# Kernel optimization log

Hardware: AMD Instinct MI355X
Metric: run time of the kernel (lower is better)

Reference implementation:

```python
import jax, jax.numpy as jnp
import numpy as np

B, L = 4096, 64
H, E, T, S = 512, 256, 256, 128
CT = T + 3            # context feature dim (term_embedding_dim + 3)
R, V = 4096, 256      # n production rules, n symbols
IN = 2 * E + 2 * T + 6 + H + S  # GRUCell input dim = 1670
NEG = -1e9


def setup_inputs() -> dict:
    key = jax.random.key(0)
    ks = jax.random.split(key, 24)
    sc = 0.02
    inp = {
        "s_tm1": jax.random.normal(ks[0], (B, H), jnp.float32),
        "a_tm1": jax.random.normal(ks[1], (B, E), jnp.float32),
        "p_t": jax.random.normal(ks[2], (B, H + E), jnp.float32),
        "symbol_idx": jax.random.randint(ks[3], (B,), 0, V, jnp.int32),
        "env_emb": jax.random.normal(ks[4], (B, L, CT), jnp.float32),
        "env_len": jax.random.randint(ks[5], (B,), 0, L, jnp.int32),
        "lc_emb": jax.random.normal(ks[6], (B, L, CT), jnp.float32),
        "lc_len": jax.random.randint(ks[7], (B,), 0, L, jnp.int32),
        # parameters
        "symbol_table": jax.random.normal(ks[8], (V, S), jnp.float32) * sc,
        "W1": jax.random.normal(ks[9], (H + CT, H), jnp.float32) * sc,
        "b1": jnp.zeros((H,), jnp.float32),
        "W2": jax.random.normal(ks[10], (H,), jnp.float32) * sc,
        "b2": jnp.zeros((), jnp.float32),
        "W_ih": jax.random.normal(ks[11], (IN, 3 * H), jnp.float32) * sc,
        "W_hh": jax.random.normal(ks[12], (H, 3 * H), jnp.float32) * sc,
        "b_ih": jnp.zeros((3 * H,), jnp.float32),
        "b_hh": jnp.zeros((3 * H,), jnp.float32),
        "Wd": jax.random.normal(ks[13], (H, E), jnp.float32) * sc,
        "bd": jnp.zeros((E,), jnp.float32),
        "rule_table": jax.random.normal(ks[14], (R, E), jnp.float32) * sc,
    }
    return inp


def _context_read(state, emb, length, W1, b1, W2, b2):
    # state: [B,H], emb: [B,L,CT], length: [B] -> context [B,CT]
    x = jnp.concatenate([jnp.broadcast_to(state[:, None, :], emb.shape[:2] + (state.shape[-1],)), emb], axis=-1)
    h = jax.nn.relu(jnp.einsum('blk,kh->blh', x, W1) + b1)      # [B,L,H]
    logit = jnp.einsum('blh,h->bl', h, W2) + b2                  # [B,L]
    mask = jnp.arange(emb.shape[1])[None, :] < length[:, None]
    logit = jnp.where(mask, logit, NEG)
    w = jax.nn.softmax(logit, axis=1)                            # [B,L]
    ctx = jnp.einsum('bl,blc->bc', w, emb)                       # [B,CT]
    # ragged empty-context samples use the zero default_context
    return jnp.where((length > 0)[:, None], ctx, 0.0)


def reference(s_tm1, a_tm1, p_t, symbol_idx, env_emb, env_len, lc_emb, lc_len,
              symbol_table, W1, b1, W2, b2, W_ih, W_hh, b_ih, b_hh, Wd, bd, rule_table):
    n_t = symbol_table[symbol_idx]                               # [B,S]
    ctx_env = _context_read(s_tm1, env_emb, env_len, W1, b1, W2, b2)
    ctx_lc = _context_read(s_tm1, lc_emb, lc_len, W1, b1, W2, b2)
    x = jnp.concatenate([a_tm1, p_t, n_t, ctx_env, ctx_lc], axis=-1)  # [B,IN]
    # torch GRUCell
    gx = x @ W_ih + b_ih                                         # [B,3H]
    gh = s_tm1 @ W_hh + b_hh
    xr, xz, xn = jnp.split(gx, 3, axis=-1)
    hr, hz, hn = jnp.split(gh, 3, axis=-1)
    r = jax.nn.sigmoid(xr + hr)
    z = jax.nn.sigmoid(xz + hz)
    n = jnp.tanh(xn + r * hn)
    h_new = (1.0 - z) * n + z * s_tm1                            # [B,H]
    dec = jnp.tanh(h_new @ Wd + bd)                              # [B,E]
    logits = dec @ rule_table.T                                  # [B,R]
    return logits
```

## Files before the change

### kernel.cpp

```cpp
#include <hip/hip_runtime.h>
#include <hip/hip_bf16.h>
#include <stdint.h>
#include <stddef.h>

#define XP 1696
#define KC 288

typedef __attribute__((ext_vector_type(8))) short bf16x8;
typedef __attribute__((ext_vector_type(4))) float f32x4;

__device__ __forceinline__ unsigned short f32_bf16(float f) {
    union { float f; unsigned int u; } v; v.f = f;
    unsigned int r = v.u + 0x7FFFu + ((v.u >> 16) & 1u);
    return (unsigned short)(r >> 16);
}
__device__ __forceinline__ float bf16_f32(unsigned short u) {
    union { unsigned int u; float f; } v; v.u = ((unsigned int)u) << 16;
    return v.f;
}

__global__ void tpack_kernel(const float* __restrict__ src, unsigned short* __restrict__ dst,
                             int Ksrc, int Nsrc, int Kp, long total) {
    long idx = (long)blockIdx.x * blockDim.x + threadIdx.x;
    if (idx >= total) return;
    int k = (int)(idx / Nsrc);
    int n = (int)(idx - (long)k * Nsrc);
    float v = (k < Ksrc) ? src[(size_t)k * Nsrc + n] : 0.0f;
    dst[(size_t)n * Kp + k] = f32_bf16(v);
}

__global__ void cvt_kernel(const float* __restrict__ src, unsigned short* __restrict__ dst, int total) {
    int idx = blockIdx.x * blockDim.x + threadIdx.x;
    if (idx < total) dst[idx] = f32_bf16(src[idx]);
}

__global__ void xasm_kernel(const float* __restrict__ a_tm1, const float* __restrict__ p_t,
                            const int* __restrict__ sym, const float* __restrict__ symtab,
                            unsigned short* __restrict__ x_out) {
    int idx = blockIdx.x * blockDim.x + threadIdx.x;
    if (idx >= 4096 * XP) return;
    int b = idx / XP, c = idx - b * XP;
    float v;
    if (c < 256)       v = a_tm1[(size_t)b * 256 + c];
    else if (c < 1024) v = p_t[(size_t)b * 768 + (c - 256)];
    else if (c < 1152) v = symtab[(size_t)sym[b] * 128 + (c - 1024)];
    else if (c < 1670) return;
    else v = 0.0f;
    x_out[idx] = f32_bf16(v);
}

template<int ACT, int OUT_BF16>
__global__ __launch_bounds__(256, 2)
void gemm_bt_kernel(const unsigned short* __restrict__ A,
                    const unsigned short* __restrict__ BT,
                    const float* __restrict__ bias,
                    void* __restrict__ Cout,
                    int M, int N, int K)
{
    __shared__ unsigned short a_lds[128 * 32];
    __shared__ unsigned short b_lds[128 * 32];
    const int tid  = threadIdx.x;
    const int lane = tid & 63;
    const int wave = tid >> 6;
    const int wm = wave >> 1, wn = wave & 1;
    const int row0 = blockIdx.y * 128;
    const int col0 = blockIdx.x * 128;

    f32x4 acc[4][4];
    #pragma unroll
    for (int i = 0; i < 4; i++)
        #pragma unroll
        for (int j = 0; j < 4; j++) acc[i][j] = (f32x4){0.f, 0.f, 0.f, 0.f};

    const int fr = lane & 15;
    const int kk = (lane >> 4) * 8;
    const int srow = (lane >> 2);
    const int scol = (lane & 3) * 8;

    for (int k0 = 0; k0 < K; k0 += 32) {
        __syncthreads();
        #pragma unroll
        for (int j = 0; j < 4; j++) {
            const int c = (wave & 1) * 4 + j;
            const unsigned short* gsrc;
            unsigned short* ldst;
            if (wave < 2) {
                gsrc = A  + (size_t)(row0 + c * 16 + srow) * K + k0 + scol;
                ldst = &a_lds[c * 512];
            } else {
                gsrc = BT + (size_t)(col0 + c * 16 + srow) * K + k0 + scol;
                ldst = &b_lds[c * 512];
            }
            __builtin_amdgcn_global_load_lds(
                (const __attribute__((address_space(1))) void*)gsrc,
                (__attribute__((address_space(3))) void*)ldst, 16, 0, 0);
        }
        __syncthreads();

        bf16x8 af[4], bf[4];
        #pragma unroll
        for (int mt = 0; mt < 4; mt++) af[mt] = *(const bf16x8*)&a_lds[(wm * 64 + mt * 16 + fr) * 32 + kk];
        #pragma unroll
        for (int nt = 0; nt < 4; nt++) bf[nt] = *(const bf16x8*)&b_lds[(wn * 64 + nt * 16 + fr) * 32 + kk];
        #pragma unroll
        for (int mt = 0; mt < 4; mt++)
            #pragma unroll
            for (int nt = 0; nt < 4; nt++)
                acc[mt][nt] = __builtin_amdgcn_mfma_f32_16x16x32_bf16(af[mt], bf[nt], acc[mt][nt], 0, 0, 0);
    }

    const int fq = lane >> 4;
    #pragma unroll
    for (int mt = 0; mt < 4; mt++)
        #pragma unroll
        for (int nt = 0; nt < 4; nt++) {
            int cg = col0 + wn * 64 + nt * 16 + fr;
            float bv = bias ? bias[cg] : 0.0f;
            #pragma unroll
            for (int i = 0; i < 4; i++) {
                int rg = row0 + wm * 64 + mt * 16 + fq * 4 + i;
                float v = acc[mt][nt][i] + bv;
                if (ACT == 1) v = tanhf(v);
                if (OUT_BF16) ((unsigned short*)Cout)[(size_t)rg * N + cg] = f32_bf16(v);
                else          ((float*)Cout)[(size_t)rg * N + cg] = v;
            }
        }
}

__global__ __launch_bounds__(512, 4)
void ctx_kernel(const float* __restrict__ emb_env, const float* __restrict__ emb_lc,
                const int* __restrict__ len_env, const int* __restrict__ len_lc,
                const float* __restrict__ s_proj,
                const unsigned short* __restrict__ W1eT,
                const float* __restrict__ W2, const float* __restrict__ b2,
                unsigned short* __restrict__ x_out)
{
    const int b = blockIdx.x;
    const int which = blockIdx.y;
    const float* emb = (which ? emb_lc : emb_env) + (size_t)b * (64 * 259);
    const int len = (which ? len_lc : len_env)[b];
    const int xoff = which ? 1411 : 1152;

    const int tid = threadIdx.x;

    if (len == 0) {
        for (int c = tid; c < 259; c += 512)
            x_out[(size_t)b * XP + xoff + c] = 0;
        return;
    }

    __shared__ unsigned short emb_lds[64][296];
    __shared__ float partial_lds[8][64];
    __shared__ float w_lds[64];

    const int mtiles = (len + 15) >> 4;

    for (int q = tid; q < 64 * 37; q += 512) {
        int r = q / 37, c = 259 + (q - r * 37);
        emb_lds[r][c] = 0;
    }

    {
        const int nf4 = (len * 259 + 3) >> 2;
        const float4* emb4 = reinterpret_cast<const float4*>(emb);
        float4 v[9];
        #pragma unroll
        for (int j = 0; j < 9; j++) {
            int q = tid + j * 512;
            if (q < nf4) v[j] = emb4[q];
        }
        #pragma unroll
        for (int j = 0; j < 9; j++) {
            int q = tid + j * 512;
            if (q < nf4) {
                float fv[4] = {v[j].x, v[j].y, v[j].z, v[j].w};
                int e0 = q * 4;
                #pragma unroll
                for (int jj = 0; jj < 4; jj++) {
                    int e = e0 + jj;
                    int r = e / 259;
                    int c = e - r * 259;
                    emb_lds[r][c] = f32_bf16(fv[jj]);
                }
            }
        }
    }

    const int lane = tid & 63;
    const int wave = tid >> 6;
    const int fr = lane & 15;
    const int fq = lane >> 4;

    float wv[4];
    #pragma unroll
    for (int nt = 0; nt < 4; nt++) wv[nt] = W2[wave * 64 + nt * 16 + fr];
    const float b2v = b2[0];

    __syncthreads();

    f32x4 acc[4][4];
    #pragma unroll
    for (int i = 0; i < 4; i++)
        #pragma unroll
        for (int j = 0; j < 4; j++) acc[i][j] = (f32x4){0.f, 0.f, 0.f, 0.f};

    #pragma unroll
    for (int ks = 0; ks < 9; ks++) {
        bf16x8 bfr[4];
        #pragma unroll
        for (int nt = 0; nt < 4; nt++) {
            int n = wave * 64 + nt * 16 + fr;
            bfr[nt] = *(const bf16x8*)(W1eT + (size_t)n * KC + ks * 32 + fq * 8);
        }
        bf16x8 af[4];
        #pragma unroll
        for (int mt = 0; mt < 4; mt++)
            if (mt < mtiles)
                af[mt] = *(const bf16x8*)&emb_lds[mt * 16 + fr][ks * 32 + fq * 8];
        __builtin_amdgcn_s_setprio(1);
        #pragma unroll
        for (int nt = 0; nt < 4; nt++)
            #pragma unroll
            for (int mt = 0; mt < 4; mt++)
                if (mt < mtiles)
                    acc[mt][nt] = __builtin_amdgcn_mfma_f32_16x16x32_bf16(af[mt], bfr[nt], acc[mt][nt], 0, 0, 0);
        __builtin_amdgcn_s_setprio(0);
    }

    float plog[4][4];
    #pragma unroll
    for (int mt = 0; mt < 4; mt++)
        #pragma unroll
        for (int ii = 0; ii < 4; ii++) plog[mt][ii] = 0.f;
    #pragma unroll
    for (int nt = 0; nt < 4; nt++) {
        int n = wave * 64 + nt * 16 + fr;
        float sp = s_proj[(size_t)b * 512 + n];
        #pragma unroll
        for (int mt = 0; mt < 4; mt++)
            if (mt < mtiles)
                #pragma unroll
                for (int ii = 0; ii < 4; ii++) {
                    float h = acc[mt][nt][ii] + sp;
                    h = fmaxf(h, 0.f);
                    plog[mt][ii] += h * wv[nt];
                }
    }
    #pragma unroll
    for (int mt = 0; mt < 4; mt++)
        if (mt < mtiles)
            #pragma unroll
            for (int ii = 0; ii < 4; ii++) {
                float v = plog[mt][ii];
                v += __shfl_xor(v, 1); v += __shfl_xor(v, 2);
                v += __shfl_xor(v, 4); v += __shfl_xor(v, 8);
                if (fr == 0) partial_lds[wave][mt * 16 + fq * 4 + ii] = v;
            }
    __syncthreads();

    if (tid < 64) {
        float logit;
        if (tid < len) {
            logit = b2v;
            #pragma unroll
            for (int w = 0; w < 8; w++) logit += partial_lds[w][tid];
        } else {
            logit = -1e9f;
        }
        float m = logit;
        #pragma unroll
        for (int off = 1; off < 64; off <<= 1) m = fmaxf(m, __shfl_xor(m, off));
        float e = __expf(logit - m);
        float s = e;
        #pragma unroll
        for (int off = 1; off < 64; off <<= 1) s += __shfl_xor(s, off);
        w_lds[tid] = e / s;
    }
    __syncthreads();

    if (tid < 259) {
        const int c = tid;
        float a0 = 0.f, a1 = 0.f, a2 = 0.f, a3 = 0.f;
        int l = 0;
        for (; l + 3 < len; l += 4) {
            a0 += w_lds[l]     * bf16_f32(emb_lds[l][c]);
            a1 += w_lds[l + 1] * bf16_f32(emb_lds[l + 1][c]);
            a2 += w_lds[l + 2] * bf16_f32(emb_lds[l + 2][c]);
            a3 += w_lds[l + 3] * bf16_f32(emb_lds[l + 3][c]);
        }
        for (; l < len; l++) a0 += w_lds[l] * bf16_f32(emb_lds[l][c]);
        x_out[(size_t)b * XP + xoff + c] = f32_bf16((a0 + a1) + (a2 + a3));
    }
}

__global__ void gru_kernel(const float* __restrict__ gx, const float* __restrict__ gh,
                           const float* __restrict__ s, unsigned short* __restrict__ h_b) {
    int idx = blockIdx.x * blockDim.x + threadIdx.x;
    if (idx >= 4096 * 512) return;
    int b = idx >> 9, c = idx & 511;
    const float* gxb = gx + (size_t)b * 1536;
    const float* ghb = gh + (size_t)b * 1536;
    float xr = gxb[c], xz = gxb[c + 512], xn = gxb[c + 1024];
    float hr = ghb[c], hz = ghb[c + 512], hn = ghb[c + 1024];
    float r = 1.f / (1.f + __expf(-(xr + hr)));
    float z = 1.f / (1.f + __expf(-(xz + hz)));
    float n = tanhf(xn + r * hn);
    float h = (1.f - z) * n + z * s[idx];
    h_b[idx] = f32_bf16(h);
}

extern "C" void kernel_launch(void* const* d_in, const int* in_sizes, int n_in,
                              void* d_out, int out_size, void* d_ws, size_t ws_size,
                              hipStream_t stream) {
    const float* s_tm1   = (const float*)d_in[0];
    const float* a_tm1   = (const float*)d_in[1];
    const float* p_t     = (const float*)d_in[2];
    const int*   sym     = (const int*)d_in[3];
    const float* env_emb = (const float*)d_in[4];
    const int*   env_len = (const int*)d_in[5];
    const float* lc_emb  = (const float*)d_in[6];
    const int*   lc_len  = (const int*)d_in[7];
    const float* symtab  = (const float*)d_in[8];
    const float* W1      = (const float*)d_in[9];
    const float* b1      = (const float*)d_in[10];
    const float* W2      = (const float*)d_in[11];
    const float* b2      = (const float*)d_in[12];
    const float* W_ih    = (const float*)d_in[13];
    const float* W_hh    = (const float*)d_in[14];
    const float* b_ih    = (const float*)d_in[15];
    const float* b_hh    = (const float*)d_in[16];
    const float* Wd      = (const float*)d_in[17];
    const float* bd      = (const float*)d_in[18];
    const float* rule    = (const float*)d_in[19];

    char* w = (char*)d_ws;
    float* s_proj = (float*)w;              w += (size_t)4096 * 512 * 4;
    unsigned short* W1sT  = (unsigned short*)w; w += (size_t)512 * 512 * 2;
    unsigned short* W1eT  = (unsigned short*)w; w += (size_t)512 * KC * 2;
    unsigned short* WihT  = (unsigned short*)w; w += (size_t)1536 * XP * 2;
    unsigned short* WhhT  = (unsigned short*)w; w += (size_t)1536 * 512 * 2;
    unsigned short* WdT   = (unsigned short*)w; w += (size_t)256 * 512 * 2;
    unsigned short* ruleb = (unsigned short*)w; w += (size_t)4096 * 256 * 2;
    unsigned short* s_b   = (unsigned short*)w; w += (size_t)4096 * 512 * 2;
    unsigned short* x_b   = (unsigned short*)w; w += (size_t)4096 * XP * 2;
    unsigned short* h_b   = (unsigned short*)w; w += (size_t)4096 * 512 * 2;
    unsigned short* dec_b = (unsigned short*)w; w += (size_t)4096 * 256 * 2;

    float* out_f = (float*)d_out;
    float* gx = out_f;
    float* gh = out_f + (size_t)4096 * 1536;

    tpack_kernel<<<(512 * 512 + 255) / 256, 256, 0, stream>>>(W1, W1sT, 512, 512, 512, (long)512 * 512);
    tpack_kernel<<<(512 * KC + 255) / 256, 256, 0, stream>>>(W1 + (size_t)512 * 512, W1eT, 259, 512, KC, (long)512 * KC);
    tpack_kernel<<<(1536 * XP + 255) / 256, 256, 0, stream>>>(W_ih, WihT, 1670, 1536, XP, (long)1536 * XP);
    tpack_kernel<<<(1536 * 512 + 255) / 256, 256, 0, stream>>>(W_hh, WhhT, 512, 1536, 512, (long)1536 * 512);
    tpack_kernel<<<(256 * 512 + 255) / 256, 256, 0, stream>>>(Wd, WdT, 512, 256, 512, (long)256 * 512);
    cvt_kernel<<<4096, 256, 0, stream>>>(rule, ruleb, 4096 * 256);
    cvt_kernel<<<8192, 256, 0, stream>>>(s_tm1, s_b, 4096 * 512);
    xasm_kernel<<<(4096 * XP + 255) / 256, 256, 0, stream>>>(a_tm1, p_t, sym, symtab, x_b);

    gemm_bt_kernel<0, 0><<<dim3(4, 32), 256, 0, stream>>>(s_b, W1sT, b1, s_proj, 4096, 512, 512);

    ctx_kernel<<<dim3(4096, 2), 512, 0, stream>>>(env_emb, lc_emb, env_len, lc_len,
                                                  s_proj, W1eT, W2, b2, x_b);

    gemm_bt_kernel<0, 0><<<dim3(12, 32), 256, 0, stream>>>(x_b, WihT, b_ih, gx, 4096, 1536, XP);
    gemm_bt_kernel<0, 0><<<dim3(12, 32), 256, 0, stream>>>(s_b, WhhT, b_hh, gh, 4096, 1536, 512);
    gru_kernel<<<8192, 256, 0, stream>>>(gx, gh, s_tm1, h_b);

    gemm_bt_kernel<1, 1><<<dim3(2, 32), 256, 0, stream>>>(h_b, WdT, bd, dec_b, 4096, 256, 512);

    gemm_bt_kernel<0, 0><<<dim3(32, 32), 256, 0, stream>>>(dec_b, ruleb, nullptr, out_f, 4096, 4096, 256);
}
```

Before: 446.7 us.

## Bin-pack ragged context sequences into shared 64-row MFMA tiles

Adds a scheduling pass that groups (batch, env/lc) context reads by their number of 16-row tiles. Up to four short sequences, or two medium ones, share one ctx_kernel block's 64-row MFMA tile, while long ones get a block to themselves. The aim is to cut the number of blocks, the redundant per-block W1e weight fetches and the idle MFMA work on partially filled tiles. In exchange it adds two small kernels with atomics, an indirection through a slot table, and full-tile MFMA work even on padded rows.

```diff
diff --git a/kernel.cpp b/kernel.cpp
--- a/kernel.cpp
+++ b/kernel.cpp
@@ -5,6 +5,12 @@
 
 #define XP 1696
 #define KC 288
+
+#define BIG_G   8192
+#define TWO_G   4096
+#define ONE_G   2048
+#define N_GROUP (BIG_G + TWO_G + ONE_G)
+#define N_SLOTI (N_GROUP * 4)
 
 typedef __attribute__((ext_vector_type(8))) short bf16x8;
 typedef __attribute__((ext_vector_type(4))) float f32x4;
@@ -47,6 +53,29 @@
     else if (c < 1670) return;
     else v = 0.0f;
     x_out[idx] = f32_bf16(v);
+}
+
+__global__ void sinit_kernel(int* __restrict__ s) {
+    int i = blockIdx.x * 256 + threadIdx.x;
+    if (i < N_SLOTI) s[i] = -1;
+    else if (i < N_SLOTI + 3) s[i] = 0;
+}
+
+__global__ void sched_kernel(const int* __restrict__ len_env, const int* __restrict__ len_lc,
+                             int* __restrict__ slots) {
+    int idx = blockIdx.x * blockDim.x + threadIdx.x;
+    if (idx >= 8192) return;
+    int b = idx >> 1, wh = idx & 1;
+    int len = wh ? len_lc[b] : len_env[b];
+    int m = (len + 15) >> 4;
+    if (m == 0) m = 1;
+    if (m > 4) m = 4;
+    int* cursors = slots + N_SLOTI;
+    int base;
+    if (m >= 3)      { int p = atomicAdd(&cursors[0], 1); base = p * 4; }
+    else if (m == 2) { int p = atomicAdd(&cursors[1], 1); base = BIG_G * 4 + (p >> 1) * 4 + (p & 1) * 2; }
+    else             { int p = atomicAdd(&cursors[2], 1); base = (BIG_G + TWO_G) * 4 + (p >> 2) * 4 + (p & 3); }
+    for (int k = 0; k < m; k++) slots[base + k] = idx * 4 + k;
 }
 
 template<int ACT, int OUT_BF16>
@@ -133,45 +162,60 @@
                 const float* __restrict__ s_proj,
                 const unsigned short* __restrict__ W1eT,
                 const float* __restrict__ W2, const float* __restrict__ b2,
+                const int* __restrict__ slots,
                 unsigned short* __restrict__ x_out)
 {
-    const int b = blockIdx.x;
-    const int which = blockIdx.y;
-    const float* emb = (which ? emb_lc : emb_env) + (size_t)b * (64 * 259);
-    const int len = (which ? len_lc : len_env)[b];
-    const int xoff = which ? 1411 : 1152;
-
-    const int tid = threadIdx.x;
-
-    if (len == 0) {
-        for (int c = tid; c < 259; c += 512)
-            x_out[(size_t)b * XP + xoff + c] = 0;
-        return;
-    }
+    const int g = blockIdx.x;
+    const int4 dv = *reinterpret_cast<const int4*>(slots + (size_t)g * 4);
+    if (dv.x < 0) return;
+    int d[4] = {dv.x, dv.y, dv.z, dv.w};
 
     __shared__ unsigned short emb_lds[64][296];
     __shared__ float partial_lds[8][64];
     __shared__ float w_lds[64];
 
-    const int mtiles = (len + 15) >> 4;
-
-    for (int q = tid; q < 64 * 37; q += 512) {
-        int r = q / 37, c = 259 + (q - r * 37);
-        emb_lds[r][c] = 0;
-    }
+    const int tid = threadIdx.x;
+    const int lane = tid & 63;
+    const int wave = tid >> 6;
+    const int fr = lane & 15;
+    const int fq = lane >> 4;
+    const float b2v = b2[0];
 
     {
-        const int nf4 = (len * 259 + 3) >> 2;
-        const float4* emb4 = reinterpret_cast<const float4*>(emb);
+        const int sl = tid >> 7;
+        const int t  = tid & 127;
+        const int ds = d[sl];
+        int nrows = 0;
+        const float* src = nullptr;
+        if (ds >= 0) {
+            int it = ds >> 2, tix = ds & 3;
+            int b = it >> 1, wh = it & 1;
+            int len = (wh ? len_lc : len_env)[b];
+            nrows = len - tix * 16;
+            if (nrows > 16) nrows = 16;
+            if (nrows < 0) nrows = 0;
+            src = (wh ? emb_lc : emb_env) + ((size_t)b * 64 + tix * 16) * 259;
+        }
+        for (int q = t; q < 16 * 37; q += 128) {
+            int r = q / 37, c = 259 + (q - (q / 37) * 37);
+            emb_lds[sl * 16 + r][c] = 0;
+        }
+        const int ndead = (16 - nrows) * 259;
+        for (int q = t; q < ndead; q += 128) {
+            int r = nrows + q / 259, c = q - (q / 259) * 259;
+            emb_lds[sl * 16 + r][c] = 0;
+        }
+        const int nf4 = (nrows * 259 + 3) >> 2;
+        const float4* s4 = reinterpret_cast<const float4*>(src);
         float4 v[9];
         #pragma unroll
         for (int j = 0; j < 9; j++) {
-            int q = tid + j * 512;
-            if (q < nf4) v[j] = emb4[q];
+            int q = t + j * 128;
+            if (q < nf4) v[j] = s4[q];
         }
         #pragma unroll
         for (int j = 0; j < 9; j++) {
-            int q = tid + j * 512;
+            int q = t + j * 128;
             if (q < nf4) {
                 float fv[4] = {v[j].x, v[j].y, v[j].z, v[j].w};
                 int e0 = q * 4;
@@ -180,22 +224,11 @@
                     int e = e0 + jj;
                     int r = e / 259;
                     int c = e - r * 259;
-                    emb_lds[r][c] = f32_bf16(fv[jj]);
+                    emb_lds[sl * 16 + r][c] = f32_bf16(fv[jj]);
                 }
             }
         }
     }
-
-    const int lane = tid & 63;
-    const int wave = tid >> 6;
-    const int fr = lane & 15;
-    const int fq = lane >> 4;
-
-    float wv[4];
-    #pragma unroll
-    for (int nt = 0; nt < 4; nt++) wv[nt] = W2[wave * 64 + nt * 16 + fr];
-    const float b2v = b2[0];
-
     __syncthreads();
 
     f32x4 acc[4][4];
@@ -215,17 +248,23 @@
         bf16x8 af[4];
         #pragma unroll
         for (int mt = 0; mt < 4; mt++)
-            if (mt < mtiles)
-                af[mt] = *(const bf16x8*)&emb_lds[mt * 16 + fr][ks * 32 + fq * 8];
+            af[mt] = *(const bf16x8*)&emb_lds[mt * 16 + fr][ks * 32 + fq * 8];
         __builtin_amdgcn_s_setprio(1);
         #pragma unroll
         for (int nt = 0; nt < 4; nt++)
             #pragma unroll
             for (int mt = 0; mt < 4; mt++)
-                if (mt < mtiles)
-                    acc[mt][nt] = __builtin_amdgcn_mfma_f32_16x16x32_bf16(af[mt], bfr[nt], acc[mt][nt], 0, 0, 0);
+                acc[mt][nt] = __builtin_amdgcn_mfma_f32_16x16x32_bf16(af[mt], bfr[nt], acc[mt][nt], 0, 0, 0);
         __builtin_amdgcn_s_setprio(0);
     }
+
+    int bslot[4];
+    #pragma unroll
+    for (int mt = 0; mt < 4; mt++) bslot[mt] = d[mt] >= 0 ? (d[mt] >> 3) : -1;
+
+    float wv[4];
+    #pragma unroll
+    for (int nt = 0; nt < 4; nt++) wv[nt] = W2[wave * 64 + nt * 16 + fr];
 
     float plog[4][4];
     #pragma unroll
@@ -235,61 +274,78 @@
     #pragma unroll
     for (int nt = 0; nt < 4; nt++) {
         int n = wave * 64 + nt * 16 + fr;
-        float sp = s_proj[(size_t)b * 512 + n];
-        #pragma unroll
-        for (int mt = 0; mt < 4; mt++)
-            if (mt < mtiles)
+        #pragma unroll
+        for (int mt = 0; mt < 4; mt++) {
+            if (bslot[mt] < 0) continue;
+            float sp = s_proj[(size_t)bslot[mt] * 512 + n];
+            #pragma unroll
+            for (int ii = 0; ii < 4; ii++) {
+                float h = acc[mt][nt][ii] + sp;
+                h = fmaxf(h, 0.f);
+                plog[mt][ii] += h * wv[nt];
+            }
+        }
+    }
+    #pragma unroll
+    for (int mt = 0; mt < 4; mt++) {
+        if (bslot[mt] < 0) continue;
+        #pragma unroll
+        for (int ii = 0; ii < 4; ii++) {
+            float v = plog[mt][ii];
+            v += __shfl_xor(v, 1); v += __shfl_xor(v, 2);
+            v += __shfl_xor(v, 4); v += __shfl_xor(v, 8);
+            if (fr == 0) partial_lds[wave][mt * 16 + fq * 4 + ii] = v;
+        }
+    }
+    __syncthreads();
+
+    if (wave < 4) {
+        int dh = d[wave];
+        if (dh >= 0 && (dh & 3) == 0) {
+            int it = dh >> 2;
+            int b = it >> 1, wh = it & 1;
+            int len = (wh ? len_lc : len_env)[b];
+            int m = (len + 15) >> 4; if (m == 0) m = 1;
+            float logit = -1e9f;
+            if (lane < 16 * m && lane < len) {
+                logit = b2v;
                 #pragma unroll
-                for (int ii = 0; ii < 4; ii++) {
-                    float h = acc[mt][nt][ii] + sp;
-                    h = fmaxf(h, 0.f);
-                    plog[mt][ii] += h * wv[nt];
-                }
-    }
-    #pragma unroll
-    for (int mt = 0; mt < 4; mt++)
-        if (mt < mtiles)
-            #pragma unroll
-            for (int ii = 0; ii < 4; ii++) {
-                float v = plog[mt][ii];
-                v += __shfl_xor(v, 1); v += __shfl_xor(v, 2);
-                v += __shfl_xor(v, 4); v += __shfl_xor(v, 8);
-                if (fr == 0) partial_lds[wave][mt * 16 + fq * 4 + ii] = v;
-            }
+                for (int w = 0; w < 8; w++) logit += partial_lds[w][wave * 16 + lane];
+            }
+            float mx = logit;
+            #pragma unroll
+            for (int off = 1; off < 64; off <<= 1) mx = fmaxf(mx, __shfl_xor(mx, off));
+            float e = __expf(logit - mx);
+            float s = e;
+            #pragma unroll
+            for (int off = 1; off < 64; off <<= 1) s += __shfl_xor(s, off);
+            if (lane < 16 * m) w_lds[wave * 16 + lane] = e / s;
+        }
+    }
     __syncthreads();
 
-    if (tid < 64) {
-        float logit;
-        if (tid < len) {
-            logit = b2v;
-            #pragma unroll
-            for (int w = 0; w < 8; w++) logit += partial_lds[w][tid];
-        } else {
-            logit = -1e9f;
-        }
-        float m = logit;
-        #pragma unroll
-        for (int off = 1; off < 64; off <<= 1) m = fmaxf(m, __shfl_xor(m, off));
-        float e = __expf(logit - m);
-        float s = e;
-        #pragma unroll
-        for (int off = 1; off < 64; off <<= 1) s += __shfl_xor(s, off);
-        w_lds[tid] = e / s;
-    }
-    __syncthreads();
-
-    if (tid < 259) {
-        const int c = tid;
-        float a0 = 0.f, a1 = 0.f, a2 = 0.f, a3 = 0.f;
-        int l = 0;
-        for (; l + 3 < len; l += 4) {
-            a0 += w_lds[l]     * bf16_f32(emb_lds[l][c]);
-            a1 += w_lds[l + 1] * bf16_f32(emb_lds[l + 1][c]);
-            a2 += w_lds[l + 2] * bf16_f32(emb_lds[l + 2][c]);
-            a3 += w_lds[l + 3] * bf16_f32(emb_lds[l + 3][c]);
-        }
-        for (; l < len; l++) a0 += w_lds[l] * bf16_f32(emb_lds[l][c]);
-        x_out[(size_t)b * XP + xoff + c] = f32_bf16((a0 + a1) + (a2 + a3));
+    #pragma unroll
+    for (int g4 = 0; g4 < 4; g4++) {
+        int dh = d[g4];
+        if (dh < 0 || (dh & 3) != 0) continue;
+        int it = dh >> 2;
+        int b = it >> 1, wh = it & 1;
+        int len = (wh ? len_lc : len_env)[b];
+        int xoff = wh ? 1411 : 1152;
+        if (tid < 259) {
+            const int c = tid;
+            const int base = g4 * 16;
+            float a0 = 0.f, a1 = 0.f, a2 = 0.f, a3 = 0.f;
+            int l = 0;
+            for (; l + 3 < len; l += 4) {
+                a0 += w_lds[base + l]     * bf16_f32(emb_lds[base + l][c]);
+                a1 += w_lds[base + l + 1] * bf16_f32(emb_lds[base + l + 1][c]);
+                a2 += w_lds[base + l + 2] * bf16_f32(emb_lds[base + l + 2][c]);
+                a3 += w_lds[base + l + 3] * bf16_f32(emb_lds[base + l + 3][c]);
+            }
+            for (; l < len; l++) a0 += w_lds[base + l] * bf16_f32(emb_lds[base + l][c]);
+            x_out[(size_t)b * XP + xoff + c] = f32_bf16((a0 + a1) + (a2 + a3));
+        }
     }
 }
 
@@ -345,10 +401,14 @@
     unsigned short* x_b   = (unsigned short*)w; w += (size_t)4096 * XP * 2;
     unsigned short* h_b   = (unsigned short*)w; w += (size_t)4096 * 512 * 2;
     unsigned short* dec_b = (unsigned short*)w; w += (size_t)4096 * 256 * 2;
+    int* slots = (int*)w;                   w += (size_t)(N_SLOTI + 8) * 4;
 
     float* out_f = (float*)d_out;
     float* gx = out_f;
     float* gh = out_f + (size_t)4096 * 1536;
+
+    sinit_kernel<<<(N_SLOTI + 3 + 255) / 256, 256, 0, stream>>>(slots);
+    sched_kernel<<<32, 256, 0, stream>>>(env_len, lc_len, slots);
 
     tpack_kernel<<<(512 * 512 + 255) / 256, 256, 0, stream>>>(W1, W1sT, 512, 512, 512, (long)512 * 512);
     tpack_kernel<<<(512 * KC + 255) / 256, 256, 0, stream>>>(W1 + (size_t)512 * 512, W1eT, 259, 512, KC, (long)512 * KC);
@@ -361,8 +421,8 @@
 
     gemm_bt_kernel<0, 0><<<dim3(4, 32), 256, 0, stream>>>(s_b, W1sT, b1, s_proj, 4096, 512, 512);
 
-    ctx_kernel<<<dim3(4096, 2), 512, 0, stream>>>(env_emb, lc_emb, env_len, lc_len,
-                                                  s_proj, W1eT, W2, b2, x_b);
+    ctx_kernel<<<N_GROUP, 512, 0, stream>>>(env_emb, lc_emb, env_len, lc_len,
+                                            s_proj, W1eT, W2, b2, slots, x_b);
 
     gemm_bt_kernel<0, 0><<<dim3(12, 32), 256, 0, stream>>>(x_b, WihT, b_ih, gx, 4096, 1536, XP);
     gemm_bt_kernel<0, 0><<<dim3(12, 32), 256, 0, stream>>>(s_b, WhhT, b_hh, gh, 4096, 1536, 512);
```

After: 439.1 us. Within noise of the previous version (-1.7%).
